# Optimization experiments

Hardware: AMD Instinct MI355X
Metric: run time of the kernel (lower is better)

The kernel has to match this reference:

```python
import jax, jax.numpy as jnp
import numpy as np
from jax import lax

SINKHORN_ITERS = 20


def sinkhorn_knopp(logits, tau=1.0, iterations=SINKHORN_ITERS):
    # logits: [N, K]. Log-domain alternating row/col normalization.
    N, K = logits.shape
    P = logits / tau
    log_target_col_sum = jnp.log(jnp.asarray(N / K, dtype=logits.dtype) + 1e-9)

    def step(P, _):
        P = P - jax.nn.logsumexp(P, axis=1, keepdims=True)   # row sums -> 1
        P = P - jax.nn.logsumexp(P, axis=0, keepdims=True) + log_target_col_sum  # col sums -> N/K
        return P, None

    P, _ = lax.scan(step, P, None, length=iterations)
    return jnp.exp(P)


def setup_inputs() -> dict:
    key = jax.random.key(0)
    ks = jax.random.split(key, 8)
    N, C, K, B = 200000, 128, 32, 16
    x = jax.random.normal(ks[0], (N, C), dtype=jnp.float32)
    batch = jnp.sort(jax.random.randint(ks[1], (N,), 0, B))
    # assign_mlp: Linear(C,C) -> ReLU -> Linear(C,K)
    W1 = jax.random.normal(ks[2], (C, C), dtype=jnp.float32) / np.sqrt(C)
    b1 = jnp.zeros((C,), dtype=jnp.float32)
    W2 = jax.random.normal(ks[3], (C, K), dtype=jnp.float32) / np.sqrt(C)
    b2 = jnp.zeros((K,), dtype=jnp.float32)
    scaling = jnp.asarray(5.0, dtype=jnp.float32)
    return {"x": x, "batch": batch, "W1": W1, "b1": b1, "W2": W2, "b2": b2,
            "scaling": scaling, "num_graphs": B}


def reference(x, batch, W1, b1, W2, b2, scaling, num_graphs):
    # assignment logits: MLP(x) * scaling  -> [N, K]
    h = jax.nn.relu(x @ W1 + b1)
    logits = (h @ W2 + b2) * scaling
    # doubly-stochastic soft assignment via Sinkhorn-Knopp (tau=1.0, 20 iters)
    s = sinkhorn_knopp(logits, tau=1.0, iterations=SINKHORN_ITERS)  # [N, K]
    # pooled super-node features: scatter-sum over graphs of s[n,k]*x[n,c]
    onehot = jax.nn.one_hot(batch, num_graphs, dtype=x.dtype)        # [N, B]
    out = jnp.einsum('nb,nk,nc->bkc', onehot, s, x)                  # [B, K, C]
    return out
```

## Files before the change

kernel.cpp:

```cpp
#include <hip/hip_runtime.h>
#include <hip/hip_bf16.h>

#define C_DIM 128
#define K_DIM 32
#define N_ITERS 20
#define NSHARD 16
#define WPAD 136

typedef __attribute__((ext_vector_type(8))) short short8;
typedef __attribute__((ext_vector_type(4))) float f32x4;
typedef __attribute__((ext_vector_type(4))) unsigned short us4;

__device__ __forceinline__ unsigned short f2bf(float f) {
    __hip_bfloat16 h = __float2bfloat16(f);
    return *reinterpret_cast<unsigned short*>(&h);
}

__global__ void init_kernel(float* __restrict__ out, int n_out,
                            float* __restrict__ zreg, int n_z,
                            const float* __restrict__ W1, const float* __restrict__ W2,
                            unsigned short* __restrict__ W1t,
                            unsigned short* __restrict__ W2t) {
    int i = blockIdx.x * blockDim.x + threadIdx.x;
    int stride = gridDim.x * blockDim.x;
    for (int j = i; j < n_out; j += stride) out[j] = 0.f;
    for (int j = i; j < n_z; j += stride) zreg[j] = 0.f;
    for (int j = i; j < C_DIM * C_DIM; j += stride) {
        int n = j >> 7, k = j & 127;
        W1t[j] = f2bf(W1[k * C_DIM + n]);
    }
    for (int j = i; j < C_DIM * K_DIM; j += stride) {
        int n = j >> 7, k = j & 127;
        W2t[j] = f2bf(W2[k * K_DIM + n]);
    }
}

__global__ __launch_bounds__(256, 4) void mlp_kernel(
    const float* __restrict__ x, const unsigned short* __restrict__ W1t,
    const float* __restrict__ b1, const unsigned short* __restrict__ W2t,
    const float* __restrict__ b2, const float* __restrict__ scal,
    float* __restrict__ Lg, int N, int ntiles) {
    __shared__ unsigned short sW1[C_DIM][WPAD];
    __shared__ unsigned short sW2[K_DIM][WPAD];
    __shared__ unsigned short sX[64][WPAD];
    __shared__ unsigned short sH[4][16][WPAD];
    __shared__ float sB1[C_DIM];
    __shared__ float sB2[K_DIM];

    const int tid = threadIdx.x;
    for (int i = tid; i < C_DIM * 16; i += 256) {
        const int r = i >> 4, c8 = (i & 15) * 8;
        *(float4*)&sW1[r][c8] = *(const float4*)&W1t[r * C_DIM + c8];
    }
    for (int i = tid; i < K_DIM * 16; i += 256) {
        const int r = i >> 4, c8 = (i & 15) * 8;
        *(float4*)&sW2[r][c8] = *(const float4*)&W2t[r * C_DIM + c8];
    }
    if (tid < C_DIM) sB1[tid] = b1[tid];
    if (tid < K_DIM) sB2[tid] = b2[tid];
    const float sc = *scal;

    const int wave = tid >> 6;
    const int lane = tid & 63;
    const int lr = lane & 15;
    const int kg = lane >> 4;
    __syncthreads();

    for (int tile = blockIdx.x; tile < ntiles; tile += gridDim.x) {
        const int row0 = tile * 64;
        __syncthreads();
        for (int i = tid; i < 2048; i += 256) {
            const int r = i >> 5, c4 = (i & 31) * 4;
            const float4 v = *(const float4*)&x[(size_t)(row0 + r) * C_DIM + c4];
            us4 u;
            u.x = f2bf(v.x); u.y = f2bf(v.y); u.z = f2bf(v.z); u.w = f2bf(v.w);
            *(us4*)&sX[r][c4] = u;
        }
        __syncthreads();

        short8 a[4];
#pragma unroll
        for (int kt = 0; kt < 4; ++kt)
            a[kt] = *(const short8*)&sX[wave * 16 + lr][kt * 32 + kg * 8];
#pragma unroll
        for (int ct = 0; ct < 8; ++ct) {
            const float bv = sB1[ct * 16 + lr];
            f32x4 acc = {bv, bv, bv, bv};
#pragma unroll
            for (int kt = 0; kt < 4; ++kt) {
                const short8 b = *(const short8*)&sW1[ct * 16 + lr][kt * 32 + kg * 8];
                acc = __builtin_amdgcn_mfma_f32_16x16x32_bf16(a[kt], b, acc, 0, 0, 0);
            }
#pragma unroll
            for (int r = 0; r < 4; ++r)
                sH[wave][kg * 4 + r][ct * 16 + lr] = f2bf(fmaxf(acc[r], 0.f));
        }
        __syncthreads();

        short8 a2[4];
#pragma unroll
        for (int kt = 0; kt < 4; ++kt)
            a2[kt] = *(const short8*)&sH[wave][lr][kt * 32 + kg * 8];
#pragma unroll
        for (int ct = 0; ct < 2; ++ct) {
            const float bv = sB2[ct * 16 + lr];
            f32x4 acc = {bv, bv, bv, bv};
#pragma unroll
            for (int kt = 0; kt < 4; ++kt) {
                const short8 b = *(const short8*)&sW2[ct * 16 + lr][kt * 32 + kg * 8];
                acc = __builtin_amdgcn_mfma_f32_16x16x32_bf16(a2[kt], b, acc, 0, 0, 0);
            }
#pragma unroll
            for (int r = 0; r < 4; ++r) {
                const int g = row0 + wave * 16 + kg * 4 + r;
                Lg[(size_t)g * K_DIM + ct * 16 + lr] = acc[r] * sc;
            }
        }
    }
}

__device__ __forceinline__ int bitrev5(int l) {
    return ((l & 1) << 4) | ((l & 2) << 2) | (l & 4) | ((l & 8) >> 2) |
           ((l & 16) >> 4);
}

#define FOLD_STAGE(M, HALF)                                   \
    {                                                         \
        const bool hi = (lane & (M)) != 0;                    \
        _Pragma("unroll")                                     \
        for (int j = 0; j < (HALF); ++j) {                    \
            const float give = hi ? p[j] : p[j + (HALF)];     \
            const float keep = hi ? p[j + (HALF)] : p[j];     \
            p[j] = keep + __shfl_xor(give, (M));              \
        }                                                     \
    }

__global__ __launch_bounds__(1024, 4) void sinkhorn_kernel(
    float* __restrict__ Lg, float* __restrict__ shards, int* __restrict__ arrive,
    int N, int nblocks) {
    __shared__ float sv[K_DIM];
    __shared__ float swsum[16][K_DIM];
    __shared__ float sdl[K_DIM];
    const int tid = threadIdx.x;
    const int wave = tid >> 6;
    const int lane = tid & 63;
    const size_t n = (size_t)blockIdx.x * 1024 + tid;
    const bool valid = n < (size_t)N;
    const int myshard = blockIdx.x & (NSHARD - 1);
    const float log_tgt = __logf((float)N / (float)K_DIM);

    if (tid < K_DIM) sv[tid] = 0.f;

    float L[K_DIM];
    if (valid) {
        const float4* Lr = (const float4*)(Lg + n * K_DIM);
#pragma unroll
        for (int j = 0; j < 8; ++j) {
            const float4 v = Lr[j];
            L[4 * j] = v.x; L[4 * j + 1] = v.y; L[4 * j + 2] = v.z; L[4 * j + 3] = v.w;
        }
    } else {
#pragma unroll
        for (int j = 0; j < K_DIM; ++j) L[j] = 0.f;
    }
    __syncthreads();

    float m0 = 0.f, inv = 0.f;
    for (int t = 1; t <= N_ITERS; ++t) {
        float p[K_DIM];
        if (valid) {
#pragma unroll
            for (int j = 0; j < K_DIM; ++j) p[j] = L[j] - sv[j];
            m0 = p[0];
#pragma unroll
            for (int j = 1; j < K_DIM; ++j) m0 = fmaxf(m0, p[j]);
            float sum = 0.f;
#pragma unroll
            for (int j = 0; j < K_DIM; ++j) {
                p[j] = __expf(p[j] - m0);
                sum += p[j];
            }
            inv = 1.f / sum;
#pragma unroll
            for (int j = 0; j < K_DIM; ++j) p[j] *= inv;
        } else {
#pragma unroll
            for (int j = 0; j < K_DIM; ++j) p[j] = 0.f;
        }

        FOLD_STAGE(1, 16)
        FOLD_STAGE(2, 8)
        FOLD_STAGE(4, 4)
        FOLD_STAGE(8, 2)
        FOLD_STAGE(16, 1)
        const float tot = p[0] + __shfl_xor(p[0], 32);
        if (lane < K_DIM) swsum[wave][bitrev5(lane)] = tot;
        __syncthreads();
        if (tid < K_DIM) {
            float s_ = 0.f;
#pragma unroll
            for (int w = 0; w < 16; ++w) s_ += swsum[w][tid];
            atomicAdd(&shards[((size_t)t * NSHARD + myshard) * K_DIM + tid], s_);
        }
        asm volatile("s_waitcnt vmcnt(0)" ::: "memory");
        __syncthreads();
        if (tid == 0) {
            __hip_atomic_fetch_add(arrive + t, 1, __ATOMIC_RELAXED,
                                   __HIP_MEMORY_SCOPE_AGENT);
            while (__hip_atomic_load(arrive + t, __ATOMIC_RELAXED,
                                     __HIP_MEMORY_SCOPE_AGENT) < nblocks)
                __builtin_amdgcn_s_sleep(16);
        }
        __syncthreads();

        if (tid < K_DIM) {
            float cs = 0.f;
#pragma unroll
            for (int sh = 0; sh < NSHARD; ++sh)
                cs += __hip_atomic_load(
                    &shards[((size_t)t * NSHARD + sh) * K_DIM + tid],
                    __ATOMIC_RELAXED, __HIP_MEMORY_SCOPE_AGENT);
            if (t < N_ITERS)
                sv[tid] += __logf(cs) - log_tgt;
            else
                sdl[tid] = ((float)N / (float)K_DIM) / cs;
        }
        __syncthreads();
    }

    if (valid) {
        float4* Sr = (float4*)(Lg + n * K_DIM);
#pragma unroll
        for (int j = 0; j < 8; ++j) {
            float4 o;
            o.x = __expf(L[4 * j + 0] - sv[4 * j + 0] - m0) * inv * sdl[4 * j + 0];
            o.y = __expf(L[4 * j + 1] - sv[4 * j + 1] - m0) * inv * sdl[4 * j + 1];
            o.z = __expf(L[4 * j + 2] - sv[4 * j + 2] - m0) * inv * sdl[4 * j + 2];
            o.w = __expf(L[4 * j + 3] - sv[4 * j + 3] - m0) * inv * sdl[4 * j + 3];
            Sr[j] = o;
        }
    }
}

#define PCHUNK 96
#define PCH_PER_BLOCK 4

__global__ __launch_bounds__(256) void pool_kernel(
    const float* __restrict__ x, const int* __restrict__ batch,
    const float* __restrict__ Sg, float* __restrict__ out, int N) {
    __shared__ float sx[PCHUNK][C_DIM];
    __shared__ float ss[PCHUNK][K_DIM];
    __shared__ int sb[PCHUNK];

    const int tid = threadIdx.x;
    const int k0 = (tid >> 5) * 4;
    const int c0 = (tid & 31) * 4;
    float acc[4][4];
#pragma unroll
    for (int i = 0; i < 4; ++i)
#pragma unroll
        for (int j = 0; j < 4; ++j) acc[i][j] = 0.f;

    int cur_b = -1;
    const int base0 = blockIdx.x * (PCHUNK * PCH_PER_BLOCK);

    for (int cc = 0; cc < PCH_PER_BLOCK; ++cc) {
        const int base = base0 + cc * PCHUNK;
        if (base >= N) break;
        const int rows = min(PCHUNK, N - base);
        __syncthreads();
        {
            const float4* src = (const float4*)(x + (size_t)base * C_DIM);
            for (int i = tid; i < rows * (C_DIM / 4); i += 256)
                ((float4*)&sx[0][0])[i] = src[i];
            const float4* ssrc = (const float4*)(Sg + (size_t)base * K_DIM);
            for (int i = tid; i < rows * (K_DIM / 4); i += 256)
                ((float4*)&ss[0][0])[i] = ssrc[i];
        }
        if (tid < rows) sb[tid] = batch[base + tid];
        __syncthreads();

        for (int r = 0; r < rows; ++r) {
            const int b = sb[r];
            if (b != cur_b) {
                if (cur_b >= 0) {
                    float* ob = out + ((size_t)cur_b * K_DIM + k0) * C_DIM + c0;
#pragma unroll
                    for (int i = 0; i < 4; ++i)
#pragma unroll
                        for (int j = 0; j < 4; ++j) {
                            atomicAdd(&ob[i * C_DIM + j], acc[i][j]);
                            acc[i][j] = 0.f;
                        }
                }
                cur_b = b;
            }
            const float4 sv = *(const float4*)&ss[r][k0];
            const float4 xv = *(const float4*)&sx[r][c0];
            const float sA[4] = {sv.x, sv.y, sv.z, sv.w};
            const float xA[4] = {xv.x, xv.y, xv.z, xv.w};
#pragma unroll
            for (int i = 0; i < 4; ++i)
#pragma unroll
                for (int j = 0; j < 4; ++j)
                    acc[i][j] = fmaf(sA[i], xA[j], acc[i][j]);
        }
    }
    if (cur_b >= 0) {
        float* ob = out + ((size_t)cur_b * K_DIM + k0) * C_DIM + c0;
#pragma unroll
        for (int i = 0; i < 4; ++i)
#pragma unroll
            for (int j = 0; j < 4; ++j) atomicAdd(&ob[i * C_DIM + j], acc[i][j]);
    }
}

extern "C" void kernel_launch(void* const* d_in, const int* in_sizes, int n_in,
                              void* d_out, int out_size, void* d_ws, size_t ws_size,
                              hipStream_t stream) {
    const float* x = (const float*)d_in[0];
    const int* batch = (const int*)d_in[1];
    const float* W1 = (const float*)d_in[2];
    const float* b1 = (const float*)d_in[3];
    const float* W2 = (const float*)d_in[4];
    const float* b2 = (const float*)d_in[5];
    const float* scal = (const float*)d_in[6];
    float* out = (float*)d_out;

    const int N = in_sizes[1];

    float* Lg = (float*)d_ws;
    float* shards = Lg + (size_t)N * K_DIM;
    const int n_shard_f = (N_ITERS + 1) * NSHARD * K_DIM;
    int* arrive = (int*)(shards + n_shard_f);
    unsigned short* W1t = (unsigned short*)(arrive + 64);
    unsigned short* W2t = W1t + C_DIM * C_DIM;

    init_kernel<<<64, 256, 0, stream>>>(out, out_size, shards, n_shard_f + 64,
                                        W1, W2, W1t, W2t);

    const int ntiles = N / 64;
    mlp_kernel<<<640, 256, 0, stream>>>(x, W1t, b1, W2t, b2, scal, Lg, N, ntiles);

    const int sblocks = (N + 1023) / 1024;
    sinkhorn_kernel<<<sblocks, 1024, 0, stream>>>(Lg, shards, arrive, N, sblocks);

    const int pblocks = (N + PCHUNK * PCH_PER_BLOCK - 1) / (PCHUNK * PCH_PER_BLOCK);
    pool_kernel<<<pblocks, 256, 0, stream>>>(x, batch, Lg, out, N);
}
```

Before: 486.2 us.

## Use last-arriver grid barrier and one Sinkhorn block per CU

The Sinkhorn kernel now launches a fixed 256 blocks of 832 threads (13 waves), so every CU holds one block. The per-iteration grid barrier is also restructured. The last block to arrive sums the shard partials, computes the column correction once and publishes it to a global vector plus a done flag. The other blocks spin on that flag with a shorter sleep and read the single published value, instead of all blocks polling the arrive counter and each re-reading all shards. This cuts redundant shard loads and contention on the arrive counter, but adds a serial reduction by one block to each iteration's critical path.

```diff
diff --git a/kernel.cpp b/kernel.cpp
--- a/kernel.cpp
+++ b/kernel.cpp
@@ -6,6 +6,8 @@
 #define N_ITERS 20
 #define NSHARD 16
 #define WPAD 136
+#define SK_THREADS 832
+#define SK_WAVES 13
 
 typedef __attribute__((ext_vector_type(8))) short short8;
 typedef __attribute__((ext_vector_type(4))) float f32x4;
@@ -135,16 +137,18 @@
         }                                                     \
     }
 
-__global__ __launch_bounds__(1024, 4) void sinkhorn_kernel(
-    float* __restrict__ Lg, float* __restrict__ shards, int* __restrict__ arrive,
+__global__ __launch_bounds__(SK_THREADS) void sinkhorn_kernel(
+    float* __restrict__ Lg, float* __restrict__ shards,
+    float* __restrict__ vglob, int* __restrict__ arrive, int* __restrict__ done,
     int N, int nblocks) {
     __shared__ float sv[K_DIM];
-    __shared__ float swsum[16][K_DIM];
+    __shared__ float swsum[SK_WAVES][K_DIM];
     __shared__ float sdl[K_DIM];
+    __shared__ int is_last;
     const int tid = threadIdx.x;
     const int wave = tid >> 6;
     const int lane = tid & 63;
-    const size_t n = (size_t)blockIdx.x * 1024 + tid;
+    const size_t n = (size_t)blockIdx.x * SK_THREADS + tid;
     const bool valid = n < (size_t)N;
     const int myshard = blockIdx.x & (NSHARD - 1);
     const float log_tgt = __logf((float)N / (float)K_DIM);
@@ -199,31 +203,49 @@
         if (tid < K_DIM) {
             float s_ = 0.f;
 #pragma unroll
-            for (int w = 0; w < 16; ++w) s_ += swsum[w][tid];
+            for (int w = 0; w < SK_WAVES; ++w) s_ += swsum[w][tid];
             atomicAdd(&shards[((size_t)t * NSHARD + myshard) * K_DIM + tid], s_);
         }
         asm volatile("s_waitcnt vmcnt(0)" ::: "memory");
         __syncthreads();
         if (tid == 0) {
-            __hip_atomic_fetch_add(arrive + t, 1, __ATOMIC_RELAXED,
+            const int old = __hip_atomic_fetch_add(arrive + t, 1, __ATOMIC_RELAXED,
+                                                   __HIP_MEMORY_SCOPE_AGENT);
+            is_last = (old == nblocks - 1);
+        }
+        __syncthreads();
+        if (is_last) {
+            if (tid < K_DIM) {
+                float cs = 0.f;
+#pragma unroll
+                for (int sh = 0; sh < NSHARD; ++sh)
+                    cs += __hip_atomic_load(
+                        &shards[((size_t)t * NSHARD + sh) * K_DIM + tid],
+                        __ATOMIC_RELAXED, __HIP_MEMORY_SCOPE_AGENT);
+                const float v = (t < N_ITERS) ? (__logf(cs) - log_tgt)
+                                              : ((float)N / (float)K_DIM) / cs;
+                __hip_atomic_store(&vglob[t * K_DIM + tid], v, __ATOMIC_RELAXED,
                                    __HIP_MEMORY_SCOPE_AGENT);
-            while (__hip_atomic_load(arrive + t, __ATOMIC_RELAXED,
-                                     __HIP_MEMORY_SCOPE_AGENT) < nblocks)
-                __builtin_amdgcn_s_sleep(16);
-        }
-        __syncthreads();
-
+            }
+            asm volatile("s_waitcnt vmcnt(0)" ::: "memory");
+            __syncthreads();
+            if (tid == 0)
+                __hip_atomic_store(done + t, 1, __ATOMIC_RELAXED,
+                                   __HIP_MEMORY_SCOPE_AGENT);
+        } else {
+            if (tid == 0) {
+                while (__hip_atomic_load(done + t, __ATOMIC_RELAXED,
+                                         __HIP_MEMORY_SCOPE_AGENT) == 0)
+                    __builtin_amdgcn_s_sleep(2);
+            }
+        }
+        __syncthreads();
         if (tid < K_DIM) {
-            float cs = 0.f;
-#pragma unroll
-            for (int sh = 0; sh < NSHARD; ++sh)
-                cs += __hip_atomic_load(
-                    &shards[((size_t)t * NSHARD + sh) * K_DIM + tid],
-                    __ATOMIC_RELAXED, __HIP_MEMORY_SCOPE_AGENT);
-            if (t < N_ITERS)
-                sv[tid] += __logf(cs) - log_tgt;
-            else
-                sdl[tid] = ((float)N / (float)K_DIM) / cs;
+            const float v = __hip_atomic_load(&vglob[t * K_DIM + tid],
+                                              __ATOMIC_RELAXED,
+                                              __HIP_MEMORY_SCOPE_AGENT);
+            if (t < N_ITERS) sv[tid] += v;
+            else sdl[tid] = v;
         }
         __syncthreads();
     }
@@ -333,17 +355,22 @@
     float* shards = Lg + (size_t)N * K_DIM;
     const int n_shard_f = (N_ITERS + 1) * NSHARD * K_DIM;
     int* arrive = (int*)(shards + n_shard_f);
-    unsigned short* W1t = (unsigned short*)(arrive + 64);
+    int* done = arrive + 32;
+    float* vglob = (float*)(done + 32);
+    const int n_vglob = (N_ITERS + 1) * K_DIM;
+    unsigned short* W1t = (unsigned short*)(vglob + n_vglob);
     unsigned short* W2t = W1t + C_DIM * C_DIM;
-
-    init_kernel<<<64, 256, 0, stream>>>(out, out_size, shards, n_shard_f + 64,
+    const int n_z = n_shard_f + 64 + n_vglob;
+
+    init_kernel<<<64, 256, 0, stream>>>(out, out_size, shards, n_z,
                                         W1, W2, W1t, W2t);
 
     const int ntiles = N / 64;
     mlp_kernel<<<640, 256, 0, stream>>>(x, W1t, b1, W2t, b2, scal, Lg, N, ntiles);
 
-    const int sblocks = (N + 1023) / 1024;
-    sinkhorn_kernel<<<sblocks, 1024, 0, stream>>>(Lg, shards, arrive, N, sblocks);
+    const int sblocks = 256;
+    sinkhorn_kernel<<<sblocks, SK_THREADS, 0, stream>>>(Lg, shards, vglob,
+                                                        arrive, done, N, sblocks);
 
     const int pblocks = (N + PCHUNK * PCH_PER_BLOCK - 1) / (PCHUNK * PCH_PER_BLOCK);
     pool_kernel<<<pblocks, 256, 0, stream>>>(x, batch, Lg, out, N);
```

Measured after the change: 491.1 us. About the same (+1.0%).
